# Kernel tuning notes

Hardware: AMD Instinct MI355X
Metric: run time of the kernel (lower is better)

The kernel has to match this reference:

```python
import jax, jax.numpy as jnp
import numpy as np

V, B, S, D, VOCAB = 2, 8, 2048, 512, 8192
STEPS = 16
DECAY = 0.999
EPS = 1e-6


def _rms(x):
    return x * jax.lax.rsqrt(jnp.mean(x * x, axis=-1, keepdims=True) + EPS)


def _phi(x):  # elu_plus_1 feature map
    return jax.nn.elu(x) + 1.0


def setup_inputs() -> dict:
    key = jax.random.key(0)
    ks = jax.random.split(key, 11)
    sc = 0.02
    return {
        "inputs": jax.random.randint(ks[0], (B, S), 0, VOCAB),
        "emb": jax.random.normal(ks[1], (V, VOCAB, D), jnp.float32) * sc,
        "Wg": jax.random.normal(ks[2], (D, D), jnp.float32) * sc,
        "Wu": jax.random.normal(ks[3], (D, 2 * D), jnp.float32) * sc,
        "Wd": jax.random.normal(ks[4], (2 * D, D), jnp.float32) * sc,
        "Wq": jax.random.normal(ks[5], (D, D), jnp.float32) * sc,
        "Wk": jax.random.normal(ks[6], (D, D), jnp.float32) * sc,
        "Wv": jax.random.normal(ks[7], (D, D), jnp.float32) * sc,
        "Wo": jax.random.normal(ks[8], (D, D), jnp.float32) * sc,
        "Wlm": jax.random.normal(ks[9], (D, VOCAB), jnp.float32) * sc,
        "recurrence_steps": STEPS,
        "adaptive_floor": 0,
    }


def reference(inputs, emb, Wg, Wu, Wd, Wq, Wk, Wv, Wo, Wlm,
              recurrence_steps, adaptive_floor):
    # adaptive_floor is unused in cross_token_mode='fused'.
    v, vocab, d = emb.shape
    b, s = inputs.shape
    inv_sqrt_d = np.float32(1.0 / np.sqrt(d))
    inv_s = np.float32(1.0 / max(s, 1))

    # [V, B, S, D] -> fold views into batch: [V*B, S, D]
    state0 = emb[:, inputs].reshape(v * b, s, d)
    acc0 = jnp.zeros((v * b, d, d), state0.dtype)

    def step(carry, _):
        state, acc = carry
        # gated MLP recurrent block (residual, step_size=1, exact gelu)
        n = _rms(state)
        gate = jax.nn.sigmoid(n @ Wg)
        cand = jax.nn.gelu(n @ Wu, approximate=False) @ Wd
        state = state + gate * cand
        # fused mixer: decaying linear-attention accumulator
        n2 = _rms(state)
        q = _phi(n2 @ Wq)
        k = _phi(n2 @ Wk)
        val = n2 @ Wv
        step_acc = jnp.einsum("bsd,bse->bde", k, val) * inv_s
        acc = DECAY * acc + step_acc
        mixed = jnp.einsum("bsd,bde->bse", q, acc) * inv_sqrt_d
        state = state + mixed @ Wo
        return (state, acc), None

    (state, _), _ = jax.lax.scan(step, (state0, acc0), None,
                                 length=int(recurrence_steps))

    combined = state.reshape(v, b, s, d).mean(axis=0)  # average view combine
    logits = _rms(combined) @ Wlm  # [B, S, VOCAB]
    return logits
```

## Files before the change

### kernel.cpp

```cpp
#include <hip/hip_runtime.h>
#include <math.h>

#define V_   2
#define B_   8
#define S_   2048
#define D_   512
#define VOCAB_ 8192
#define STEPS_ 16
#define DECAY_ 0.999f
#define EPS_ 1e-6f
#define VB_  (V_ * B_)
#define R_   (VB_ * S_)
#define RD_  ((long)R_ * D_)

typedef unsigned int u32;
typedef __attribute__((ext_vector_type(8)))  short bf16x8;
typedef __attribute__((ext_vector_type(16))) float f32x16;

enum Act { ACT_IDENT = 0, ACT_SIGMOID = 1, ACT_GELU = 2, ACT_PHI = 3 };

template <int ACT>
__device__ __forceinline__ float act_fn(float x) {
    if (ACT == ACT_SIGMOID) return 1.0f / (1.0f + __expf(-x));
    if (ACT == ACT_GELU)    return 0.5f * x * (1.0f + erff(x * 0.70710678118654752f));
    if (ACT == ACT_PHI)     return x > 0.0f ? x + 1.0f : __expf(x);
    return x;
}

__device__ __forceinline__ void split3(float x, u32& h, u32& m, u32& l) {
    u32 bx = __float_as_uint(x);
    u32 hb = bx & 0xFFFF0000u;
    float r = x - __uint_as_float(hb);
    u32 rb = __float_as_uint(r);
    u32 mb = rb & 0xFFFF0000u;
    float r2 = r - __uint_as_float(mb);
    h = hb >> 16;
    m = mb >> 16;
    l = __float_as_uint(r2) >> 16;
}


template <bool TRANS_A>
__device__ __forceinline__ void load_tile(const float* __restrict__ A,
                                          const float* __restrict__ Bm,
                                          int M, int N, int K,
                                          int rowBase, int colBase, int k0, int t,
                                          float4 (&av)[4], float4 (&bv)[4]) {
    if (!TRANS_A) {
#pragma unroll
        for (int i = 0; i < 4; i++) {
            const int id = i * 256 + t;
            const int m = id >> 3, kq = id & 7;
            av[i] = *(const float4*)&A[(long)(rowBase + m) * K + k0 + kq * 4];
        }
    } else {
#pragma unroll
        for (int i = 0; i < 4; i++) {
            const int id = i * 256 + t;
            const int kq = id >> 7, m = id & 127;
            const float* p0 = &A[(long)(k0 + kq * 4) * M + rowBase + m];
            av[i].x = p0[0]; av[i].y = p0[M]; av[i].z = p0[2 * M]; av[i].w = p0[3 * M];
        }
    }
#pragma unroll
    for (int i = 0; i < 4; i++) {
        const int id = i * 256 + t;
        const int kq = id >> 7, n = id & 127;
        const float* p0 = &Bm[(long)(k0 + kq * 4) * N + colBase + n];
        bv[i].x = p0[0]; bv[i].y = p0[N]; bv[i].z = p0[2 * N]; bv[i].w = p0[3 * N];
    }
}

__device__ __forceinline__ void stage_quad(u32* base, int row, int kq, float4 v) {
    u32 h0, m0, l0, h1, m1, l1, h2, m2, l2, h3, m3, l3;
    split3(v.x, h0, m0, l0); split3(v.y, h1, m1, l1);
    split3(v.z, h2, m2, l2); split3(v.w, h3, m3, l3);
    const int sw = ((kq >> 1) ^ (row & 3) ^ ((row >> 2) & 3));
    u32* p = base + row * 16 + sw * 4 + (kq & 1) * 2;
    p[0]    = h0 | (h1 << 16); p[1]    = h2 | (h3 << 16);
    p[2048] = m0 | (m1 << 16); p[2049] = m2 | (m3 << 16);
    p[4096] = l0 | (l1 << 16); p[4097] = l2 | (l3 << 16);
}

template <int ACT, bool HAS_GATE, bool TRANS_A>
__launch_bounds__(256)
__global__ void gemm_mfma(const float* __restrict__ A, const float* __restrict__ Bm,
                          float* __restrict__ C, const float* __restrict__ Gate,
                          int M, int N, int K,
                          long sA, long sB, long sC,
                          float alpha, float beta) {
    __shared__ u32 lds[12288];
    const int bz = blockIdx.z;
    A  += (long)bz * sA;
    Bm += (long)bz * sB;
    C  += (long)bz * sC;
    const int colBase = blockIdx.x * 128;
    const int rowBase = blockIdx.y * 128;
    const int t    = threadIdx.x;
    const int lane = t & 63;
    const int w    = t >> 6;
    const int wm   = (w >> 1) * 64;
    const int wn   = (w & 1) * 64;
    const int l31  = lane & 31;
    const int lg   = lane >> 5;

    f32x16 acc[2][2];
#pragma unroll
    for (int a = 0; a < 2; a++)
#pragma unroll
        for (int b = 0; b < 2; b++)
#pragma unroll
            for (int r = 0; r < 16; r++) acc[a][b][r] = 0.0f;

    float4 av[4], bv[4];
    load_tile<TRANS_A>(A, Bm, M, N, K, rowBase, colBase, 0, t, av, bv);

    for (int k0 = 0; k0 < K; k0 += 32) {
        __syncthreads();
#pragma unroll
        for (int i = 0; i < 4; i++) {
            const int id = i * 256 + t;
            int row, kq;
            if (!TRANS_A) { row = id >> 3; kq = id & 7; }
            else          { kq = id >> 7; row = id & 127; }
            stage_quad(lds, row, kq, av[i]);
        }
#pragma unroll
        for (int i = 0; i < 4; i++) {
            const int id = i * 256 + t;
            const int kq = id >> 7, n = id & 127;
            stage_quad(lds + 6144, n, kq, bv[i]);
        }
        __syncthreads();

        if (k0 + 32 < K)
            load_tile<TRANS_A>(A, Bm, M, N, K, rowBase, colBase, k0 + 32, t, av, bv);

        bf16x8 af[2][2][3];
#pragma unroll
        for (int at = 0; at < 2; at++) {
            const int m  = wm + at * 32 + l31;
            const int sx = (m & 3) ^ ((m >> 2) & 3);
#pragma unroll
            for (int kh = 0; kh < 2; kh++) {
                const int c = kh * 2 + lg;
#pragma unroll
                for (int p = 0; p < 3; p++)
                    af[at][kh][p] = *(const bf16x8*)&lds[p * 2048 + m * 16 + ((c ^ sx) << 2)];
            }
        }
#pragma unroll
        for (int bt = 0; bt < 2; bt++) {
            const int n  = wn + bt * 32 + l31;
            const int sx = (n & 3) ^ ((n >> 2) & 3);
            bf16x8 bf[2][3];
#pragma unroll
            for (int kh = 0; kh < 2; kh++) {
                const int c = kh * 2 + lg;
#pragma unroll
                for (int p = 0; p < 3; p++)
                    bf[kh][p] = *(const bf16x8*)&lds[6144 + p * 2048 + n * 16 + ((c ^ sx) << 2)];
            }
#define DO_PROD(pa, pb)                                                        \
    _Pragma("unroll")                                                          \
    for (int at = 0; at < 2; at++)                                             \
        _Pragma("unroll")                                                      \
        for (int kh = 0; kh < 2; kh++)                                         \
            acc[at][bt] = __builtin_amdgcn_mfma_f32_32x32x16_bf16(             \
                af[at][kh][pa], bf[kh][pb], acc[at][bt], 0, 0, 0);
            DO_PROD(0, 0) DO_PROD(0, 1) DO_PROD(1, 0) DO_PROD(1, 1)
            DO_PROD(0, 2) DO_PROD(2, 0) DO_PROD(1, 2) DO_PROD(2, 1)
#undef DO_PROD
        }
    }

#pragma unroll
    for (int at = 0; at < 2; at++)
#pragma unroll
        for (int bt = 0; bt < 2; bt++) {
            const long gc = colBase + wn + bt * 32 + l31;
#pragma unroll
            for (int r = 0; r < 16; r++) {
                const long gr = rowBase + wm + at * 32 + (r & 3) + 8 * (r >> 2) + 4 * lg;
                const long idx = gr * (long)N + gc;
                float vx = alpha * act_fn<ACT>(acc[at][bt][r]);
                if (HAS_GATE) vx *= Gate[idx];
                if (beta != 0.0f) vx += beta * C[idx];
                C[idx] = vx;
            }
        }
}

__launch_bounds__(128)
__global__ void rms_kernel(const float* __restrict__ X, float* __restrict__ Y) {
    const long row = blockIdx.x;
    const float4 v = *(const float4*)&X[row * D_ + threadIdx.x * 4];
    float ss = v.x * v.x + v.y * v.y + v.z * v.z + v.w * v.w;
#pragma unroll
    for (int off = 32; off > 0; off >>= 1) ss += __shfl_down(ss, off, 64);
    __shared__ float s2[2];
    if ((threadIdx.x & 63) == 0) s2[threadIdx.x >> 6] = ss;
    __syncthreads();
    const float tot = s2[0] + s2[1];
    const float sc = rsqrtf(tot * (1.0f / (float)D_) + EPS_);
    float4 o;
    o.x = v.x * sc; o.y = v.y * sc; o.z = v.z * sc; o.w = v.w * sc;
    *(float4*)&Y[row * D_ + threadIdx.x * 4] = o;
}

__launch_bounds__(128)
__global__ void embed_kernel(const int* __restrict__ inputs, const float* __restrict__ emb,
                             float* __restrict__ state) {
    const int row = blockIdx.x;
    const int s  = row & (S_ - 1);
    const int vb = row >> 11;
    const int b  = vb & (B_ - 1);
    const int v  = vb >> 3;
    const int tok = inputs[b * S_ + s];
    const float4 val = *(const float4*)&emb[((long)v * VOCAB_ + tok) * D_ + threadIdx.x * 4];
    *(float4*)&state[(long)row * D_ + threadIdx.x * 4] = val;
}

__launch_bounds__(256)
__global__ void combine_kernel(const float* __restrict__ state, float* __restrict__ comb) {
    const long i = (long)blockIdx.x * 256 + threadIdx.x;
    const float4 a = ((const float4*)state)[i];
    const float4 c = ((const float4*)(state + (long)B_ * S_ * D_))[i];
    float4 o;
    o.x = 0.5f * (a.x + c.x); o.y = 0.5f * (a.y + c.y);
    o.z = 0.5f * (a.z + c.z); o.w = 0.5f * (a.w + c.w);
    ((float4*)comb)[i] = o;
}

extern "C" void kernel_launch(void* const* d_in, const int* in_sizes, int n_in,
                              void* d_out, int out_size, void* d_ws, size_t ws_size,
                              hipStream_t stream) {
    const int*   inputs = (const int*)d_in[0];
    const float* emb = (const float*)d_in[1];
    const float* Wg  = (const float*)d_in[2];
    const float* Wu  = (const float*)d_in[3];
    const float* Wd  = (const float*)d_in[4];
    const float* Wq  = (const float*)d_in[5];
    const float* Wk  = (const float*)d_in[6];
    const float* Wv  = (const float*)d_in[7];
    const float* Wv_o = (const float*)d_in[8];
    const float* Wlm = (const float*)d_in[9];
    float* out = (float*)d_out;

    float* ws    = (float*)d_ws;
    float* state = ws;
    float* nbuf  = ws + 1 * RD_;
    float* gbuf  = ws + 2 * RD_;
    float* ubuf  = ws + 3 * RD_;
    float* qbuf  = ws + 5 * RD_;
    float* kbuf  = ws + 6 * RD_;
    float* vbuf  = ws + 7 * RD_;
    float* accb  = ws + 8 * RD_;

    const float inv_s  = 1.0f / (float)S_;
    const float inv_sd = 0.044194173824159216f;

    hipMemsetAsync(accb, 0, (size_t)VB_ * D_ * D_ * sizeof(float), stream);
    embed_kernel<<<R_, 128, 0, stream>>>(inputs, emb, state);

    for (int step = 0; step < STEPS_; step++) {
        rms_kernel<<<R_, 128, 0, stream>>>(state, nbuf);
        gemm_mfma<ACT_SIGMOID, false, false><<<dim3(4, 256, 1), 256, 0, stream>>>(
            nbuf, Wg, gbuf, nullptr, R_, D_, D_, 0, 0, 0, 1.0f, 0.0f);
        gemm_mfma<ACT_GELU, false, false><<<dim3(8, 256, 1), 256, 0, stream>>>(
            nbuf, Wu, ubuf, nullptr, R_, 2 * D_, D_, 0, 0, 0, 1.0f, 0.0f);
        gemm_mfma<ACT_IDENT, true, false><<<dim3(4, 256, 1), 256, 0, stream>>>(
            ubuf, Wd, state, gbuf, R_, D_, 2 * D_, 0, 0, 0, 1.0f, 1.0f);
        rms_kernel<<<R_, 128, 0, stream>>>(state, nbuf);
        gemm_mfma<ACT_PHI, false, false><<<dim3(4, 256, 1), 256, 0, stream>>>(
            nbuf, Wq, qbuf, nullptr, R_, D_, D_, 0, 0, 0, 1.0f, 0.0f);
        gemm_mfma<ACT_PHI, false, false><<<dim3(4, 256, 1), 256, 0, stream>>>(
            nbuf, Wk, kbuf, nullptr, R_, D_, D_, 0, 0, 0, 1.0f, 0.0f);
        gemm_mfma<ACT_IDENT, false, false><<<dim3(4, 256, 1), 256, 0, stream>>>(
            nbuf, Wv, vbuf, nullptr, R_, D_, D_, 0, 0, 0, 1.0f, 0.0f);
        gemm_mfma<ACT_IDENT, false, true><<<dim3(4, 4, VB_), 256, 0, stream>>>(
            kbuf, vbuf, accb, nullptr, D_, D_, S_,
            (long)S_ * D_, (long)S_ * D_, (long)D_ * D_, inv_s, DECAY_);
        gemm_mfma<ACT_IDENT, false, false><<<dim3(4, 16, VB_), 256, 0, stream>>>(
            qbuf, accb, nbuf, nullptr, S_, D_, D_,
            (long)S_ * D_, (long)D_ * D_, (long)S_ * D_, inv_sd, 0.0f);
        gemm_mfma<ACT_IDENT, false, false><<<dim3(4, 256, 1), 256, 0, stream>>>(
            nbuf, Wv_o, state, nullptr, R_, D_, D_, 0, 0, 0, 1.0f, 1.0f);
    }

    combine_kernel<<<(B_ * S_ * D_ / 4) / 256, 256, 0, stream>>>(state, gbuf);
    rms_kernel<<<B_ * S_, 128, 0, stream>>>(gbuf, gbuf);
    gemm_mfma<ACT_IDENT, false, false><<<dim3(64, 128, 1), 256, 0, stream>>>(
        gbuf, Wlm, out, nullptr, B_ * S_, VOCAB_, D_, 0, 0, 0, 1.0f, 0.0f);
}
```

Baseline: 26.67 ms.

## Pre-split operands into bf16 planes and drop lowest-order MFMA cross terms

Adds a GEMM variant that reads operands already split into hi/mid/lo bf16 planes, with weights transposed and split once per launch and activations split inside the RMS or producer epilogues. The per-tile fp32-to-bf16x3 splitting inside the GEMM main loop goes away, and global reads shrink from fp32 to 16-bit planes. It also drops the two lowest-order product terms (mid*lo and lo*mid), cutting MFMA work from 8 to 6 terms per tile. In exchange it adds extra plane writes and memory traffic and gives slightly lower precision.

```diff
diff --git a/kernel.cpp b/kernel.cpp
--- a/kernel.cpp
+++ b/kernel.cpp
@@ -14,6 +14,7 @@
 #define RD_  ((long)R_ * D_)
 
 typedef unsigned int u32;
+typedef unsigned short u16;
 typedef __attribute__((ext_vector_type(8)))  short bf16x8;
 typedef __attribute__((ext_vector_type(16))) float f32x16;
 
@@ -39,6 +40,127 @@
     l = __float_as_uint(r2) >> 16;
 }
 
+template <int ACT, bool HAS_GATE, bool WRITE_C, bool WRITE_PLANES>
+__launch_bounds__(256)
+__global__ void gemm_pl(const u16* __restrict__ Ap, const u16* __restrict__ Bp,
+                        float* __restrict__ C, const float* __restrict__ Gate,
+                        u16* __restrict__ Pout,
+                        int M, int N, int K,
+                        long sAp, long sBp, long sPout,
+                        float alpha, float beta) {
+    __shared__ u16 lds[24576];
+    const int colBase = blockIdx.x * 128;
+    const int rowBase = blockIdx.y * 128;
+    const int t    = threadIdx.x;
+    const int lane = t & 63;
+    const int w    = t >> 6;
+    const int wm   = (w >> 1) * 64;
+    const int wn   = (w & 1) * 64;
+    const int l31  = lane & 31;
+    const int lg   = lane >> 5;
+
+    u32 goff[12];
+    int doff[12];
+#pragma unroll
+    for (int i = 0; i < 12; i++) {
+        const int id  = i * 256 + t;
+        const int op  = id / 1536;
+        const int rem = id - op * 1536;
+        const int pid = rem >> 9;
+        const int rid = rem & 511;
+        const int row = rid >> 2, c = rid & 3;
+        const int sx  = (row & 3) ^ ((row >> 2) & 3);
+        if (op == 0) goff[i] = (u32)((long)pid * sAp + (long)(rowBase + row) * K + c * 8);
+        else         goff[i] = (u32)((long)pid * sBp + (long)(colBase + row) * K + c * 8);
+        doff[i] = op * 12288 + pid * 4096 + row * 32 + ((c ^ sx) << 3);
+    }
+
+    f32x16 acc[2][2];
+#pragma unroll
+    for (int a = 0; a < 2; a++)
+#pragma unroll
+        for (int b = 0; b < 2; b++)
+#pragma unroll
+            for (int r = 0; r < 16; r++) acc[a][b][r] = 0.0f;
+
+    uint4 st[12];
+#pragma unroll
+    for (int i = 0; i < 12; i++)
+        st[i] = *(const uint4*)((i < 6 ? Ap : Bp) + goff[i]);
+
+    for (int k0 = 0; k0 < K; k0 += 32) {
+        __syncthreads();
+#pragma unroll
+        for (int i = 0; i < 12; i++) *(uint4*)&lds[doff[i]] = st[i];
+        __syncthreads();
+        if (k0 + 32 < K) {
+#pragma unroll
+            for (int i = 0; i < 12; i++)
+                st[i] = *(const uint4*)((i < 6 ? Ap : Bp) + goff[i] + (k0 + 32));
+        }
+
+        bf16x8 af[2][2][3];
+#pragma unroll
+        for (int at = 0; at < 2; at++) {
+            const int m  = wm + at * 32 + l31;
+            const int sx = (m & 3) ^ ((m >> 2) & 3);
+#pragma unroll
+            for (int kh = 0; kh < 2; kh++) {
+                const int ck = kh * 2 + lg;
+#pragma unroll
+                for (int p = 0; p < 3; p++)
+                    af[at][kh][p] = *(const bf16x8*)&lds[p * 4096 + m * 32 + (((ck ^ sx) & 3) << 3)];
+            }
+        }
+#pragma unroll
+        for (int bt = 0; bt < 2; bt++) {
+            const int n  = wn + bt * 32 + l31;
+            const int sx = (n & 3) ^ ((n >> 2) & 3);
+            bf16x8 bf[2][3];
+#pragma unroll
+            for (int kh = 0; kh < 2; kh++) {
+                const int ck = kh * 2 + lg;
+#pragma unroll
+                for (int p = 0; p < 3; p++)
+                    bf[kh][p] = *(const bf16x8*)&lds[12288 + p * 4096 + n * 32 + (((ck ^ sx) & 3) << 3)];
+            }
+#define DO_PROD(pa, pb)                                                        \
+    _Pragma("unroll")                                                          \
+    for (int at = 0; at < 2; at++)                                             \
+        _Pragma("unroll")                                                      \
+        for (int kh = 0; kh < 2; kh++)                                         \
+            acc[at][bt] = __builtin_amdgcn_mfma_f32_32x32x16_bf16(             \
+                af[at][kh][pa], bf[kh][pb], acc[at][bt], 0, 0, 0);
+            DO_PROD(0, 0) DO_PROD(0, 1) DO_PROD(1, 0) DO_PROD(1, 1)
+            DO_PROD(0, 2) DO_PROD(2, 0)
+#undef DO_PROD
+        }
+    }
+
+#pragma unroll
+    for (int at = 0; at < 2; at++)
+#pragma unroll
+        for (int bt = 0; bt < 2; bt++) {
+            const long gc = colBase + wn + bt * 32 + l31;
+#pragma unroll
+            for (int r = 0; r < 16; r++) {
+                const long gr = rowBase + wm + at * 32 + (r & 3) + 8 * (r >> 2) + 4 * lg;
+                const long idx = gr * (long)N + gc;
+                float vx = alpha * act_fn<ACT>(acc[at][bt][r]);
+                if (HAS_GATE) vx *= Gate[idx];
+                if (WRITE_C) {
+                    if (beta != 0.0f) vx += beta * C[idx];
+                    C[idx] = vx;
+                }
+                if (WRITE_PLANES) {
+                    u32 hh, mm, ll; split3(vx, hh, mm, ll);
+                    Pout[idx] = (u16)hh;
+                    Pout[sPout + idx] = (u16)mm;
+                    Pout[2 * sPout + idx] = (u16)ll;
+                }
+            }
+        }
+}
 
 template <bool TRANS_A>
 __device__ __forceinline__ void load_tile(const float* __restrict__ A,
@@ -82,18 +204,20 @@
     p[4096] = l0 | (l1 << 16); p[4097] = l2 | (l3 << 16);
 }
 
-template <int ACT, bool HAS_GATE, bool TRANS_A>
+template <int ACT, bool HAS_GATE, bool TRANS_A, bool WRITE_C, bool WRITE_PLANES>
 __launch_bounds__(256)
 __global__ void gemm_mfma(const float* __restrict__ A, const float* __restrict__ Bm,
                           float* __restrict__ C, const float* __restrict__ Gate,
+                          u16* __restrict__ Pout,
                           int M, int N, int K,
-                          long sA, long sB, long sC,
+                          long sA, long sB, long sC, long sPout,
                           float alpha, float beta) {
     __shared__ u32 lds[12288];
     const int bz = blockIdx.z;
     A  += (long)bz * sA;
     Bm += (long)bz * sB;
-    C  += (long)bz * sC;
+    if (WRITE_C)      C    += (long)bz * sC;
+    if (WRITE_PLANES) Pout += (long)bz * sC;
     const int colBase = blockIdx.x * 128;
     const int rowBase = blockIdx.y * 128;
     const int t    = threadIdx.x;
@@ -146,7 +270,7 @@
                 const int c = kh * 2 + lg;
 #pragma unroll
                 for (int p = 0; p < 3; p++)
-                    af[at][kh][p] = *(const bf16x8*)&lds[p * 2048 + m * 16 + ((c ^ sx) << 2)];
+                    af[at][kh][p] = *(const bf16x8*)&lds[p * 2048 + m * 16 + (((c ^ sx) & 3) << 2)];
             }
         }
 #pragma unroll
@@ -159,7 +283,7 @@
                 const int c = kh * 2 + lg;
 #pragma unroll
                 for (int p = 0; p < 3; p++)
-                    bf[kh][p] = *(const bf16x8*)&lds[6144 + p * 2048 + n * 16 + ((c ^ sx) << 2)];
+                    bf[kh][p] = *(const bf16x8*)&lds[6144 + p * 2048 + n * 16 + (((c ^ sx) & 3) << 2)];
             }
 #define DO_PROD(pa, pb)                                                        \
     _Pragma("unroll")                                                          \
@@ -169,7 +293,7 @@
             acc[at][bt] = __builtin_amdgcn_mfma_f32_32x32x16_bf16(             \
                 af[at][kh][pa], bf[kh][pb], acc[at][bt], 0, 0, 0);
             DO_PROD(0, 0) DO_PROD(0, 1) DO_PROD(1, 0) DO_PROD(1, 1)
-            DO_PROD(0, 2) DO_PROD(2, 0) DO_PROD(1, 2) DO_PROD(2, 1)
+            DO_PROD(0, 2) DO_PROD(2, 0)
 #undef DO_PROD
         }
     }
@@ -185,14 +309,22 @@
                 const long idx = gr * (long)N + gc;
                 float vx = alpha * act_fn<ACT>(acc[at][bt][r]);
                 if (HAS_GATE) vx *= Gate[idx];
-                if (beta != 0.0f) vx += beta * C[idx];
-                C[idx] = vx;
+                if (WRITE_C) {
+                    if (beta != 0.0f) vx += beta * C[idx];
+                    C[idx] = vx;
+                }
+                if (WRITE_PLANES) {
+                    u32 hh, mm, ll; split3(vx, hh, mm, ll);
+                    Pout[idx] = (u16)hh;
+                    Pout[sPout + idx] = (u16)mm;
+                    Pout[2 * sPout + idx] = (u16)ll;
+                }
             }
         }
 }
 
 __launch_bounds__(128)
-__global__ void rms_kernel(const float* __restrict__ X, float* __restrict__ Y) {
+__global__ void rms_split_kernel(const float* __restrict__ X, u16* __restrict__ P, long sP) {
     const long row = blockIdx.x;
     const float4 v = *(const float4*)&X[row * D_ + threadIdx.x * 4];
     float ss = v.x * v.x + v.y * v.y + v.z * v.z + v.w * v.w;
@@ -201,11 +333,37 @@
     __shared__ float s2[2];
     if ((threadIdx.x & 63) == 0) s2[threadIdx.x >> 6] = ss;
     __syncthreads();
-    const float tot = s2[0] + s2[1];
-    const float sc = rsqrtf(tot * (1.0f / (float)D_) + EPS_);
-    float4 o;
-    o.x = v.x * sc; o.y = v.y * sc; o.z = v.z * sc; o.w = v.w * sc;
-    *(float4*)&Y[row * D_ + threadIdx.x * 4] = o;
+    const float sc = rsqrtf((s2[0] + s2[1]) * (1.0f / (float)D_) + EPS_);
+    float o[4] = {v.x * sc, v.y * sc, v.z * sc, v.w * sc};
+    u32 h[4], m[4], l[4];
+#pragma unroll
+    for (int j = 0; j < 4; j++) split3(o[j], h[j], m[j], l[j]);
+    const long base = row * D_ + threadIdx.x * 4;
+    uint2 ph, pm, pl;
+    ph.x = h[0] | (h[1] << 16); ph.y = h[2] | (h[3] << 16);
+    pm.x = m[0] | (m[1] << 16); pm.y = m[2] | (m[3] << 16);
+    pl.x = l[0] | (l[1] << 16); pl.y = l[2] | (l[3] << 16);
+    *(uint2*)&P[base] = ph;
+    *(uint2*)&P[sP + base] = pm;
+    *(uint2*)&P[2 * sP + base] = pl;
+}
+
+__launch_bounds__(256)
+__global__ void wsplit_kernel(const float* __restrict__ W, u16* __restrict__ P, int K, int N) {
+    const int n  = blockIdx.y * 256 + threadIdx.x;
+    const int k0 = blockIdx.x * 4;
+    const long sP = (long)K * N;
+    u32 h[4], m[4], l[4];
+#pragma unroll
+    for (int j = 0; j < 4; j++) split3(W[(long)(k0 + j) * N + n], h[j], m[j], l[j]);
+    const long base = (long)n * K + k0;
+    uint2 ph, pm, pl;
+    ph.x = h[0] | (h[1] << 16); ph.y = h[2] | (h[3] << 16);
+    pm.x = m[0] | (m[1] << 16); pm.y = m[2] | (m[3] << 16);
+    pl.x = l[0] | (l[1] << 16); pl.y = l[2] | (l[3] << 16);
+    *(uint2*)&P[base] = ph;
+    *(uint2*)&P[sP + base] = pm;
+    *(uint2*)&P[2 * sP + base] = pl;
 }
 
 __launch_bounds__(128)
@@ -249,47 +407,67 @@
 
     float* ws    = (float*)d_ws;
     float* state = ws;
-    float* nbuf  = ws + 1 * RD_;
-    float* gbuf  = ws + 2 * RD_;
-    float* ubuf  = ws + 3 * RD_;
-    float* qbuf  = ws + 5 * RD_;
-    float* kbuf  = ws + 6 * RD_;
-    float* vbuf  = ws + 7 * RD_;
-    float* accb  = ws + 8 * RD_;
+    float* gbuf  = ws + RD_;
+    float* shr   = ws + 2 * RD_;
+    float* qbuf  = shr;
+    float* kbuf  = shr + RD_;
+    float* vbuf  = shr + 2 * RD_;
+    u16*   upl   = (u16*)shr;
+    u16*   cpl   = (u16*)shr;
+    u16*   npl   = (u16*)(ws + 5 * RD_);
+    float* accb  = ws + 5 * RD_ + (3 * RD_) / 2;
+    u16*   wpl   = (u16*)(accb + (long)VB_ * D_ * D_);
+    u16* wgT  = wpl;
+    u16* wuT  = wgT + 3L * D_ * D_;
+    u16* wdT  = wuT + 3L * D_ * 2 * D_;
+    u16* wqT  = wdT + 3L * 2 * D_ * D_;
+    u16* wkT  = wqT + 3L * D_ * D_;
+    u16* wvT  = wkT + 3L * D_ * D_;
+    u16* woT  = wvT + 3L * D_ * D_;
+    u16* wlmT = woT + 3L * D_ * D_;
 
     const float inv_s  = 1.0f / (float)S_;
     const float inv_sd = 0.044194173824159216f;
 
     hipMemsetAsync(accb, 0, (size_t)VB_ * D_ * D_ * sizeof(float), stream);
     embed_kernel<<<R_, 128, 0, stream>>>(inputs, emb, state);
+    wsplit_kernel<<<dim3(D_ / 4, D_ / 256), 256, 0, stream>>>(Wg, wgT, D_, D_);
+    wsplit_kernel<<<dim3(D_ / 4, 2 * D_ / 256), 256, 0, stream>>>(Wu, wuT, D_, 2 * D_);
+    wsplit_kernel<<<dim3(2 * D_ / 4, D_ / 256), 256, 0, stream>>>(Wd, wdT, 2 * D_, D_);
+    wsplit_kernel<<<dim3(D_ / 4, D_ / 256), 256, 0, stream>>>(Wq, wqT, D_, D_);
+    wsplit_kernel<<<dim3(D_ / 4, D_ / 256), 256, 0, stream>>>(Wk, wkT, D_, D_);
+    wsplit_kernel<<<dim3(D_ / 4, D_ / 256), 256, 0, stream>>>(Wv, wvT, D_, D_);
+    wsplit_kernel<<<dim3(D_ / 4, D_ / 256), 256, 0, stream>>>(Wv_o, woT, D_, D_);
+    wsplit_kernel<<<dim3(D_ / 4, VOCAB_ / 256), 256, 0, stream>>>(Wlm, wlmT, D_, VOCAB_);
 
     for (int step = 0; step < STEPS_; step++) {
-        rms_kernel<<<R_, 128, 0, stream>>>(state, nbuf);
-        gemm_mfma<ACT_SIGMOID, false, false><<<dim3(4, 256, 1), 256, 0, stream>>>(
-            nbuf, Wg, gbuf, nullptr, R_, D_, D_, 0, 0, 0, 1.0f, 0.0f);
-        gemm_mfma<ACT_GELU, false, false><<<dim3(8, 256, 1), 256, 0, stream>>>(
-            nbuf, Wu, ubuf, nullptr, R_, 2 * D_, D_, 0, 0, 0, 1.0f, 0.0f);
-        gemm_mfma<ACT_IDENT, true, false><<<dim3(4, 256, 1), 256, 0, stream>>>(
-            ubuf, Wd, state, gbuf, R_, D_, 2 * D_, 0, 0, 0, 1.0f, 1.0f);
-        rms_kernel<<<R_, 128, 0, stream>>>(state, nbuf);
-        gemm_mfma<ACT_PHI, false, false><<<dim3(4, 256, 1), 256, 0, stream>>>(
-            nbuf, Wq, qbuf, nullptr, R_, D_, D_, 0, 0, 0, 1.0f, 0.0f);
-        gemm_mfma<ACT_PHI, false, false><<<dim3(4, 256, 1), 256, 0, stream>>>(
-            nbuf, Wk, kbuf, nullptr, R_, D_, D_, 0, 0, 0, 1.0f, 0.0f);
-        gemm_mfma<ACT_IDENT, false, false><<<dim3(4, 256, 1), 256, 0, stream>>>(
-            nbuf, Wv, vbuf, nullptr, R_, D_, D_, 0, 0, 0, 1.0f, 0.0f);
-        gemm_mfma<ACT_IDENT, false, true><<<dim3(4, 4, VB_), 256, 0, stream>>>(
-            kbuf, vbuf, accb, nullptr, D_, D_, S_,
-            (long)S_ * D_, (long)S_ * D_, (long)D_ * D_, inv_s, DECAY_);
-        gemm_mfma<ACT_IDENT, false, false><<<dim3(4, 16, VB_), 256, 0, stream>>>(
-            qbuf, accb, nbuf, nullptr, S_, D_, D_,
-            (long)S_ * D_, (long)D_ * D_, (long)S_ * D_, inv_sd, 0.0f);
-        gemm_mfma<ACT_IDENT, false, false><<<dim3(4, 256, 1), 256, 0, stream>>>(
-            nbuf, Wv_o, state, nullptr, R_, D_, D_, 0, 0, 0, 1.0f, 1.0f);
+        rms_split_kernel<<<R_, 128, 0, stream>>>(state, npl, RD_);
+        gemm_pl<ACT_SIGMOID, false, true, false><<<dim3(4, 256), 256, 0, stream>>>(
+            npl, wgT, gbuf, nullptr, nullptr, R_, D_, D_, RD_, (long)D_ * D_, 0, 1.0f, 0.0f);
+        gemm_pl<ACT_GELU, false, false, true><<<dim3(8, 256), 256, 0, stream>>>(
+            npl, wuT, nullptr, nullptr, upl, R_, 2 * D_, D_, RD_, (long)D_ * 2 * D_, 2 * RD_, 1.0f, 0.0f);
+        gemm_pl<ACT_IDENT, true, true, false><<<dim3(4, 256), 256, 0, stream>>>(
+            upl, wdT, state, gbuf, nullptr, R_, D_, 2 * D_, 2 * RD_, (long)2 * D_ * D_, 0, 1.0f, 1.0f);
+        rms_split_kernel<<<R_, 128, 0, stream>>>(state, npl, RD_);
+        gemm_pl<ACT_PHI, false, true, false><<<dim3(4, 256), 256, 0, stream>>>(
+            npl, wqT, qbuf, nullptr, nullptr, R_, D_, D_, RD_, (long)D_ * D_, 0, 1.0f, 0.0f);
+        gemm_pl<ACT_PHI, false, true, false><<<dim3(4, 256), 256, 0, stream>>>(
+            npl, wkT, kbuf, nullptr, nullptr, R_, D_, D_, RD_, (long)D_ * D_, 0, 1.0f, 0.0f);
+        gemm_pl<ACT_IDENT, false, true, false><<<dim3(4, 256), 256, 0, stream>>>(
+            npl, wvT, vbuf, nullptr, nullptr, R_, D_, D_, RD_, (long)D_ * D_, 0, 1.0f, 0.0f);
+        gemm_mfma<ACT_IDENT, false, true, true, false><<<dim3(4, 4, VB_), 256, 0, stream>>>(
+            kbuf, vbuf, accb, nullptr, nullptr, D_, D_, S_,
+            (long)S_ * D_, (long)S_ * D_, (long)D_ * D_, 0, inv_s, DECAY_);
+        gemm_mfma<ACT_IDENT, false, false, false, true><<<dim3(4, 16, VB_), 256, 0, stream>>>(
+            qbuf, accb, nullptr, nullptr, npl, S_, D_, D_,
+            (long)S_ * D_, (long)D_ * D_, (long)S_ * D_, RD_, inv_sd, 0.0f);
+        gemm_pl<ACT_IDENT, false, true, false><<<dim3(4, 256), 256, 0, stream>>>(
+            npl, woT, state, nullptr, nullptr, R_, D_, D_, RD_, (long)D_ * D_, 0, 1.0f, 1.0f);
     }
 
     combine_kernel<<<(B_ * S_ * D_ / 4) / 256, 256, 0, stream>>>(state, gbuf);
-    rms_kernel<<<B_ * S_, 128, 0, stream>>>(gbuf, gbuf);
-    gemm_mfma<ACT_IDENT, false, false><<<dim3(64, 128, 1), 256, 0, stream>>>(
-        gbuf, Wlm, out, nullptr, B_ * S_, VOCAB_, D_, 0, 0, 0, 1.0f, 0.0f);
-}
+    rms_split_kernel<<<B_ * S_, 128, 0, stream>>>(gbuf, cpl, (long)B_ * S_ * D_);
+    gemm_pl<ACT_IDENT, false, true, false><<<dim3(64, 128), 256, 0, stream>>>(
+        cpl, wlmT, out, nullptr, nullptr, B_ * S_, VOCAB_, D_,
+        (long)B_ * S_ * D_, (long)VOCAB_ * D_, 0, 1.0f, 0.0f);
+}
```

New measurement: 57.33 ms. +114.9%, slower.
